# Kernel optimization log

Hardware: AMD Instinct MI355X
Metric: run time of the kernel (lower is better)

## Reference

```python
import jax, jax.numpy as jnp
import numpy as np

EPS = 1e-5

def _layernorm(h, g, b):
    mu = jnp.mean(h, axis=-1, keepdims=True)
    var = jnp.mean((h - mu) ** 2, axis=-1, keepdims=True)
    return (h - mu) / jnp.sqrt(var + EPS) * g + b

def _linoss_scan_im(A, dt, Bu):
    # A, dt: (N,) real; Bu: (B, L, N) complex64.
    # IM discretization of z' = -A x + B u, x' = z (LinOSS paper Eq. 3-4),
    # computed with a 2x2 block-diagonal associative (parallel) scan.
    S = 1.0 / (1.0 + dt * dt * A)  # Schur complement
    m11 = 1.0 - dt * dt * A * S
    m12 = -dt * A * S
    m21 = dt * S
    m22 = S
    fz = (m11 * dt) * Bu
    fx = (m21 * dt) * Bu
    Bt, L, N = Bu.shape
    br = lambda m: jnp.broadcast_to(m.astype(Bu.dtype), (Bt, L, N))
    elems = (br(m11), br(m12), br(m21), br(m22), fz, fx)

    def binop(ei, ej):
        a11i, a12i, a21i, a22i, bzi, bxi = ei
        a11j, a12j, a21j, a22j, bzj, bxj = ej
        return (a11j * a11i + a12j * a21i,
                a11j * a12i + a12j * a22i,
                a21j * a11i + a22j * a21i,
                a21j * a12i + a22j * a22i,
                a11j * bzi + a12j * bxi + bzj,
                a21j * bzi + a22j * bxi + bxj)

    res = jax.lax.associative_scan(binop, elems, axis=1)
    return res[5]  # x-component of the state, (B, L, N) complex

def setup_inputs():
    key = jax.random.key(0)
    ks = jax.random.split(key, 20)
    B, L, H_in, D_mod = 8, 2048, 128, 512
    s_in = np.float32(1.0 / np.sqrt(H_in))
    s_d = np.float32(1.0 / np.sqrt(D_mod))
    f32 = jnp.float32
    return {
        "x": jax.random.normal(ks[0], (B, L, H_in), f32),
        "W_in": jax.random.normal(ks[1], (D_mod, H_in), f32) * s_in,
        "b_in": jnp.zeros((D_mod,), f32),
        "W_enc": jax.random.normal(ks[2], (D_mod, D_mod), f32) * s_d,
        "b_enc": jnp.zeros((D_mod,), f32),
        "ln_g": jnp.ones((D_mod,), f32),
        "ln_b": jnp.zeros((D_mod,), f32),
        "A_diag": jax.random.uniform(ks[3], (D_mod,), f32),
        "log_steps": jax.random.normal(ks[4], (D_mod,), f32) * 0.5,
        "B_re": jax.random.normal(ks[5], (D_mod, D_mod), f32) * s_d,
        "B_im": jax.random.normal(ks[6], (D_mod, D_mod), f32) * s_d,
        "C_re": jax.random.normal(ks[7], (D_mod, D_mod), f32) * s_d,
        "C_im": jax.random.normal(ks[8], (D_mod, D_mod), f32) * s_d,
        "D": jax.random.normal(ks[9], (D_mod,), f32),
        "glu_w1": jax.random.normal(ks[10], (D_mod, D_mod), f32) * s_d,
        "glu_b1": jnp.zeros((D_mod,), f32),
        "glu_w2": jax.random.normal(ks[11], (D_mod, D_mod), f32) * s_d,
        "glu_b2": jnp.zeros((D_mod,), f32),
        "W_dec": jax.random.normal(ks[12], (D_mod, D_mod), f32) * s_d,
        "b_dec": jnp.zeros((D_mod,), f32),
        "W_out": jax.random.normal(ks[13], (H_in, D_mod), f32) * s_d,
        "b_out": jnp.zeros((H_in,), f32),
    }

def reference(x, W_in, b_in, W_enc, b_enc, ln_g, ln_b, A_diag, log_steps,
              B_re, B_im, C_re, C_im, D, glu_w1, glu_b1, glu_w2, glu_b2,
              W_dec, b_dec, W_out, b_out):
    h = x @ W_in.T + b_in                       # outer in_proj: (B, L, d)
    h = h @ W_enc.T + b_enc                     # LinOSS encoder
    skip = h
    hn = _layernorm(h, ln_g, ln_b)
    A = jax.nn.relu(A_diag)                     # nonnegative oscillator freqs
    dt = jax.nn.sigmoid(log_steps)              # per-state timestep in (0,1)
    Bc = (B_re + 1j * B_im).astype(jnp.complex64)
    Cc = (C_re + 1j * C_im).astype(jnp.complex64)
    Bu = jnp.einsum('blh,nh->bln', hn.astype(jnp.complex64), Bc)
    xs = _linoss_scan_im(A, dt, Bu)             # (B, L, N) complex
    y = jnp.einsum('bln,hn->blh', xs, Cc).real + D * hn
    y = jax.nn.gelu(y)
    y = (y @ glu_w1.T + glu_b1) * jax.nn.sigmoid(y @ glu_w2.T + glu_b2)  # GLU
    h = skip + y                                # residual (dropout = eval mode)
    h = h @ W_dec.T + b_dec                     # LinOSS decoder
    return h @ W_out.T + b_out                  # outer out_proj: (B, L, out)
```

## Files before the change

### kernel.cpp

```cpp
#include <hip/hip_runtime.h>
#include <cstddef>
#include <cstdint>
#include <math.h>

typedef _Float16 f16;
typedef f16 f16x8 __attribute__((ext_vector_type(8)));
typedef f16 f16x4 __attribute__((ext_vector_type(4)));
typedef float f32x4 __attribute__((ext_vector_type(4)));

constexpr int Bb   = 8;
constexpr int Ll   = 2048;
constexpr int Hin  = 128;
constexpr int Dm   = 512;
constexpr int Mrows = Bb * Ll;
constexpr int NC   = 32;
constexpr int CL   = Ll / NC;
constexpr int SZ1  = Bb * NC * Dm;
constexpr int SD   = 1024;

static __device__ __forceinline__ float sigmoid_f(float x) {
    return 1.f / (1.f + expf(-x));
}
static __device__ __forceinline__ float gelu_tanh_f(float x) {
    float x3 = x * x * x;
    float t  = tanhf(0.7978845608028654f * (x + 0.044715f * x3));
    return 0.5f * x * (1.f + t);
}

static __device__ __forceinline__ void gld16(const f16* g, f16* l) {
    __builtin_amdgcn_global_load_lds(
        (const __attribute__((address_space(1))) void*)g,
        (__attribute__((address_space(3))) void*)l, 16, 0, 0);
}

static __device__ __forceinline__ void hard_barrier() {
    __builtin_amdgcn_sched_barrier(0);
    asm volatile("s_barrier" ::: "memory");
    __builtin_amdgcn_sched_barrier(0);
}

struct CvtJob { const float* s; f16* d; int n; int lgL; int pitch; int off; int ilv; };
struct CvtJobs { CvtJob j[7]; };

__global__ __launch_bounds__(256) void prep_k(
    CvtJobs jobs,
    const float* __restrict__ Wenc, const float* __restrict__ Win,
    const float* __restrict__ b_in, const float* __restrict__ b_enc,
    const float* __restrict__ Wout, const float* __restrict__ Wdec,
    const float* __restrict__ b_dec, const float* __restrict__ b_out,
    const float* __restrict__ A_diag, const float* __restrict__ log_steps,
    const float* __restrict__ gb1, const float* __restrict__ gb2,
    f16* __restrict__ Wc1, float* __restrict__ bc1,
    f16* __restrict__ Wc2, float* __restrict__ bc2,
    float* __restrict__ cst, float* __restrict__ BG)
{
    const int y = blockIdx.y;
    if (y < 7) {
        const CvtJob jb = jobs.j[y];
        const int mask = (1 << jb.lgL) - 1;
        for (int i = (blockIdx.x * 256 + threadIdx.x) * 4; i < jb.n; i += 512 * 256 * 4) {
            const float4 v = *(const float4*)(jb.s + i);
            const int row = i >> jb.lgL;
            const int c   = i & mask;
            f16* dp = jb.ilv
                ? jb.d + (size_t)(((row >> 6) << 7) + (row & 63) + jb.off) * jb.pitch + c
                : jb.d + (size_t)row * jb.pitch + jb.off + c;
            f16x4 o;
            o.x = (f16)v.x; o.y = (f16)v.y; o.z = (f16)v.z; o.w = (f16)v.w;
            *(f16x4*)dp = o;
        }
    } else if (y == 7) {
        if (blockIdx.x >= 256) return;
        const int d2 = blockIdx.x * 2 + (threadIdx.x >> 7);
        const int t  = threadIdx.x & 127;
        float a0 = 0.f, a1 = 0.f, a2 = 0.f, a3 = 0.f;
        float a4 = 0.f, a5 = 0.f, a6 = 0.f, a7 = 0.f;
        const float* wr = Wenc + (size_t)d2 * Dm;
        for (int d = 0; d < Dm; d += 8) {
            a0 = fmaf(wr[d + 0], Win[(d + 0) * Hin + t], a0);
            a1 = fmaf(wr[d + 1], Win[(d + 1) * Hin + t], a1);
            a2 = fmaf(wr[d + 2], Win[(d + 2) * Hin + t], a2);
            a3 = fmaf(wr[d + 3], Win[(d + 3) * Hin + t], a3);
            a4 = fmaf(wr[d + 4], Win[(d + 4) * Hin + t], a4);
            a5 = fmaf(wr[d + 5], Win[(d + 5) * Hin + t], a5);
            a6 = fmaf(wr[d + 6], Win[(d + 6) * Hin + t], a6);
            a7 = fmaf(wr[d + 7], Win[(d + 7) * Hin + t], a7);
        }
        Wc1[d2 * Hin + t] = (f16)(((a0 + a1) + (a2 + a3)) + ((a4 + a5) + (a6 + a7)));
        if (t < 64) {
            float p = 0.f;
#pragma unroll
            for (int j = 0; j < 8; ++j)
                p = fmaf(wr[t + 64 * j], b_in[t + 64 * j], p);
#pragma unroll
            for (int off = 32; off > 0; off >>= 1) p += __shfl_down(p, off);
            if (t == 0) bc1[d2] = p + b_enc[d2];
        }
    } else if (y == 8) {
        if (blockIdx.x >= 128) return;
        const int o  = blockIdx.x;
        const int t0 = threadIdx.x * 2;
        const float* wo = Wout + (size_t)o * Dm;
        float x0 = 0.f, y0 = 0.f, x1 = 0.f, y1 = 0.f;
        float x2 = 0.f, y2 = 0.f, x3 = 0.f, y3 = 0.f;
        for (int d = 0; d < Dm; d += 4) {
            const float w0 = wo[d + 0], w1 = wo[d + 1], w2 = wo[d + 2], w3 = wo[d + 3];
            const float2 v0 = *(const float2*)(Wdec + (size_t)(d + 0) * Dm + t0);
            const float2 v1 = *(const float2*)(Wdec + (size_t)(d + 1) * Dm + t0);
            const float2 v2 = *(const float2*)(Wdec + (size_t)(d + 2) * Dm + t0);
            const float2 v3 = *(const float2*)(Wdec + (size_t)(d + 3) * Dm + t0);
            x0 = fmaf(w0, v0.x, x0); y0 = fmaf(w0, v0.y, y0);
            x1 = fmaf(w1, v1.x, x1); y1 = fmaf(w1, v1.y, y1);
            x2 = fmaf(w2, v2.x, x2); y2 = fmaf(w2, v2.y, y2);
            x3 = fmaf(w3, v3.x, x3); y3 = fmaf(w3, v3.y, y3);
        }
        Wc2[(size_t)o * Dm + t0]     = (f16)((x0 + x1) + (x2 + x3));
        Wc2[(size_t)o * Dm + t0 + 1] = (f16)((y0 + y1) + (y2 + y3));
        if (threadIdx.x < 64) {
            const int t = threadIdx.x;
            float p = 0.f;
#pragma unroll
            for (int j = 0; j < 8; ++j)
                p = fmaf(wo[t + 64 * j], b_dec[t + 64 * j], p);
#pragma unroll
            for (int off = 32; off > 0; off >>= 1) p += __shfl_down(p, off);
            if (t == 0) bc2[o] = p + b_out[o];
        }
    } else {
        const int n = blockIdx.x * 256 + threadIdx.x;
        if (blockIdx.x >= 2 || n >= Dm) return;
        const float a   = fmaxf(A_diag[n], 0.f);
        const float dt  = 1.f / (1.f + expf(-log_steps[n]));
        const float d2a = dt * dt * a;
        const float S   = 1.f / (1.f + d2a);
        const float m11 = 1.f - d2a * S;
        const float m12 = -dt * a * S;
        const float m21 = dt * S;
        const float m22 = S;
        cst[n]            = m11;
        cst[Dm + n]       = m12;
        cst[2 * Dm + n]   = m21;
        cst[3 * Dm + n]   = m22;
        cst[4 * Dm + n]   = m11 * dt;
        cst[5 * Dm + n]   = m21 * dt;
        const int j = n >> 6, loc = n & 63;
        BG[(j << 7) + loc]      = gb1[n];
        BG[(j << 7) + 64 + loc] = gb2[n];
    }
}

template <int KM, int OUTF16, int BM>
__global__ __launch_bounds__(256, 2) void gemm_mfma(
    const f16* __restrict__ A, const f16* __restrict__ W,
    const float* __restrict__ bias,
    const f16* __restrict__ EX, const float* __restrict__ DV,
    void* __restrict__ Cout, int M, int N, int K)
{
    constexpr int MR   = BM / 32;
    constexpr int AELE = BM * 64;
    constexpr int BELE = 128 * 64;
    __shared__ f16 smem[2 * (AELE + BELE)];

    const int tid = threadIdx.x;
    const int l   = tid & 63;
    const int wid = tid >> 6;
    const int wr  = wid >> 1;
    const int wc  = wid & 1;
    const int lc  = l & 15;
    const int lr  = l >> 4;
    const int row0 = blockIdx.x * BM;
    const int col0 = blockIdx.y * 128;

    const int NT = K >> 6;
    const int swz  = (l & 7) << 4;
    const int off0 = ((lr * 16) ^ swz) >> 1;
    const int off1 = ((64 + lr * 16) ^ swz) >> 1;

    f32x4 acc[MR][4];
#pragma unroll
    for (int i = 0; i < MR; ++i)
#pragma unroll
        for (int j = 0; j < 4; ++j) acc[i][j] = (f32x4){0.f, 0.f, 0.f, 0.f};

    auto stage_a = [&](f16* dst, const f16* src, int rs) {
#pragma unroll
        for (int c = 0; c < MR; ++c) {
            const int chunk = c * 256 + tid;
            const int row   = chunk >> 3;
            const int kb    = ((chunk & 7) << 4) ^ ((row & 7) << 4);
            gld16(src + (size_t)row * rs + (kb >> 1), dst + chunk * 8);
        }
    };
    auto stage_b = [&](f16* dst, const f16* src, int rs) {
#pragma unroll
        for (int c = 0; c < 4; ++c) {
            const int chunk = c * 256 + tid;
            const int row   = chunk >> 3;
            const int kb    = ((chunk & 7) << 4) ^ ((row & 7) << 4);
            gld16(src + (size_t)row * rs + (kb >> 1), dst + chunk * 8);
        }
    };
    auto compute = [&](const f16* As, const f16* Bs) {
#pragma unroll
        for (int ks = 0; ks < 2; ++ks) {
            const int off = ks ? off1 : off0;
            f16x8 aF[MR], bF[4];
#pragma unroll
            for (int mi = 0; mi < MR; ++mi)
                aF[mi] = *(const f16x8*)(As + (wr * (BM / 2) + mi * 16 + lc) * 64 + off);
#pragma unroll
            for (int ni = 0; ni < 4; ++ni)
                bF[ni] = *(const f16x8*)(Bs + (wc * 64 + ni * 16 + lc) * 64 + off);
#pragma unroll
            for (int mi = 0; mi < MR; ++mi)
#pragma unroll
                for (int ni = 0; ni < 4; ++ni)
                    acc[mi][ni] = __builtin_amdgcn_mfma_f32_16x16x32_f16(
                        aF[mi], bF[ni], acc[mi][ni], 0, 0, 0);
        }
    };

    stage_a(smem, A + (size_t)row0 * K, K);
    stage_b(smem + 2 * AELE, W + (size_t)col0 * K, K);
    int cur = 0;
    for (int kt = 0; kt < NT; ++kt) {
        if (kt + 1 < NT) {
            const int k1 = (kt + 1) << 6;
            stage_a(smem + (cur ^ 1) * AELE, A + (size_t)row0 * K + k1, K);
            stage_b(smem + 2 * AELE + (cur ^ 1) * BELE, W + (size_t)col0 * K + k1, K);
            if constexpr (MR == 2)      asm volatile("s_waitcnt vmcnt(6)" ::: "memory");
            else if constexpr (MR == 1) asm volatile("s_waitcnt vmcnt(5)" ::: "memory");
            else                        asm volatile("s_waitcnt vmcnt(8)" ::: "memory");
        } else {
            asm volatile("s_waitcnt vmcnt(0)" ::: "memory");
        }
        __builtin_amdgcn_sched_barrier(0);
        hard_barrier();
        compute(smem + cur * AELE, smem + 2 * AELE + cur * BELE);
        hard_barrier();
        cur ^= 1;
    }

    float* Cf32 = (float*)Cout;
    f16*   Cf16 = (f16*)Cout;
    if constexpr (KM == 5) {
        float* sig = (float*)smem;
        __syncthreads();
        if (wc == 1) {
#pragma unroll
            for (int mi = 0; mi < MR; ++mi)
#pragma unroll
                for (int ni = 0; ni < 4; ++ni) {
                    const int col = col0 + 64 + ni * 16 + lc;
                    const int rl0 = wr * (BM / 2) + mi * 16 + lr * 4;
                    const f32x4 v = acc[mi][ni];
#pragma unroll
                    for (int r = 0; r < 4; ++r)
                        sig[(rl0 + r) * 65 + ni * 16 + lc] = sigmoid_f(v[r] + bias[col]);
                }
        }
        __syncthreads();
        if (wc == 0) {
#pragma unroll
            for (int mi = 0; mi < MR; ++mi)
#pragma unroll
                for (int ni = 0; ni < 4; ++ni) {
                    const int cl   = ni * 16 + lc;
                    const int col  = col0 + cl;
                    const int hcol = blockIdx.y * 64 + cl;
                    const int rl0  = wr * (BM / 2) + mi * 16 + lr * 4;
                    const f32x4 v = acc[mi][ni];
#pragma unroll
                    for (int r = 0; r < 4; ++r) {
                        const int row = row0 + rl0 + r;
                        const float o = (float)EX[(size_t)row * Dm + hcol]
                                      + (v[r] + bias[col]) * sig[(rl0 + r) * 65 + cl];
                        Cf16[(size_t)row * Dm + hcol] = (f16)o;
                    }
                }
        }
        return;
    }
#pragma unroll
    for (int mi = 0; mi < MR; ++mi) {
#pragma unroll
        for (int ni = 0; ni < 4; ++ni) {
            const int col   = col0 + wc * 64 + ni * 16 + lc;
            const int rbase = row0 + wr * (BM / 2) + mi * 16 + lr * 4;
            const f32x4 v = acc[mi][ni];
            if (KM == 1) {
                const float dv = DV[col];
#pragma unroll
                for (int r = 0; r < 4; ++r) {
                    const size_t idx = (size_t)(rbase + r) * N + col;
                    const float o = gelu_tanh_f(v[r] + dv * (float)EX[idx]);
                    if (OUTF16) Cf16[idx] = (f16)o; else Cf32[idx] = o;
                }
            } else {
                const float bv = bias ? bias[col] : 0.f;
#pragma unroll
                for (int r = 0; r < 4; ++r) {
                    const float o = v[r] + bv;
                    const size_t idx = (size_t)(rbase + r) * N + col;
                    if (OUTF16) Cf16[idx] = (f16)o; else Cf32[idx] = o;
                }
            }
        }
    }
}

__global__ __launch_bounds__(256) void layernorm_f16(
    const f16* __restrict__ X, const float* __restrict__ g,
    const float* __restrict__ b, f16* __restrict__ Y)
{
    const int lane = threadIdx.x & 63;
    const int w    = threadIdx.x >> 6;
    const int row  = blockIdx.x * 4 + w;
    const size_t base = (size_t)row * Dm + lane * 8;

    const f16x8 v = *(const f16x8*)(X + base);
    float x[8];
    float s = 0.f, q = 0.f;
#pragma unroll
    for (int i = 0; i < 8; ++i) {
        x[i] = (float)v[i];
        s += x[i]; q += x[i] * x[i];
    }
#pragma unroll
    for (int off = 32; off > 0; off >>= 1) {
        s += __shfl_xor(s, off);
        q += __shfl_xor(q, off);
    }
    const float mu  = s * (1.f / 512.f);
    const float var = q * (1.f / 512.f) - mu * mu;
    const float rs  = rsqrtf(var + 1e-5f);

    const float4 g0 = *(const float4*)(g + lane * 8);
    const float4 g1 = *(const float4*)(g + lane * 8 + 4);
    const float4 b0 = *(const float4*)(b + lane * 8);
    const float4 b1 = *(const float4*)(b + lane * 8 + 4);
    const float gg[8] = {g0.x, g0.y, g0.z, g0.w, g1.x, g1.y, g1.z, g1.w};
    const float bb[8] = {b0.x, b0.y, b0.z, b0.w, b1.x, b1.y, b1.z, b1.w};
    f16x8 o;
#pragma unroll
    for (int i = 0; i < 8; ++i)
        o[i] = (f16)((x[i] - mu) * rs * gg[i] + bb[i]);
    *(f16x8*)(Y + base) = o;
}

__global__ __launch_bounds__(512) void scan_phase1(
    const f16* __restrict__ BU, const float* __restrict__ cst,
    float* __restrict__ S1)
{
    const int n = threadIdx.x;
    const int c = blockIdx.x & (NC - 1);
    const int b = blockIdx.x >> 5;
    const float m11 = cst[n],          m12 = cst[Dm + n];
    const float m21 = cst[2 * Dm + n], m22 = cst[3 * Dm + n];
    const float c1  = cst[4 * Dm + n], c2  = cst[5 * Dm + n];

    float zr = 0.f, xr = 0.f, zi = 0.f, xi = 0.f;
    const size_t base = ((size_t)b * Ll + (size_t)c * CL) * SD + n;
#pragma unroll 4
    for (int t = 0; t < CL; ++t) {
        const float br = (float)BU[base + (size_t)t * SD];
        const float bi = (float)BU[base + (size_t)t * SD + 512];
        const float zrn = fmaf(m11, zr, fmaf(m12, xr, c1 * br));
        const float xrn = fmaf(m21, zr, fmaf(m22, xr, c2 * br));
        const float zin = fmaf(m11, zi, fmaf(m12, xi, c1 * bi));
        const float xin = fmaf(m21, zi, fmaf(m22, xi, c2 * bi));
        zr = zrn; xr = xrn; zi = zin; xi = xin;
    }
    const int idx = blockIdx.x * Dm + n;
    S1[idx]            = zr;
    S1[SZ1 + idx]      = xr;
    S1[2 * SZ1 + idx]  = zi;
    S1[3 * SZ1 + idx]  = xi;
}

__global__ __launch_bounds__(256) void scan_phase2(
    const float* __restrict__ S1, const float* __restrict__ cst,
    float* __restrict__ G)
{
    const int gidx = blockIdx.x * 256 + threadIdx.x;
    const int n = gidx & (Dm - 1);
    const int b = gidx >> 9;
    const float m11 = cst[n],          m12 = cst[Dm + n];
    const float m21 = cst[2 * Dm + n], m22 = cst[3 * Dm + n];

    float p11 = 1.f, p12 = 0.f, p21 = 0.f, p22 = 1.f;
    for (int i = 0; i < CL; ++i) {
        const float q11 = m11 * p11 + m12 * p21;
        const float q12 = m11 * p12 + m12 * p22;
        const float q21 = m21 * p11 + m22 * p21;
        const float q22 = m21 * p12 + m22 * p22;
        p11 = q11; p12 = q12; p21 = q21; p22 = q22;
    }

    float gzr = 0.f, gxr = 0.f, gzi = 0.f, gxi = 0.f;
    for (int c = 0; c < NC; ++c) {
        const int idx = (b * NC + c) * Dm + n;
        G[idx]           = gzr;
        G[SZ1 + idx]     = gxr;
        G[2 * SZ1 + idx] = gzi;
        G[3 * SZ1 + idx] = gxi;
        const float szr = S1[idx],           sxr = S1[SZ1 + idx];
        const float szi = S1[2 * SZ1 + idx], sxi = S1[3 * SZ1 + idx];
        const float t1 = p11 * gzr + p12 * gxr + szr;
        const float t2 = p21 * gzr + p22 * gxr + sxr;
        const float t3 = p11 * gzi + p12 * gxi + szi;
        const float t4 = p21 * gzi + p22 * gxi + sxi;
        gzr = t1; gxr = t2; gzi = t3; gxi = t4;
    }
}

__global__ __launch_bounds__(512) void scan_phase3(
    const f16* __restrict__ BU, const float* __restrict__ cst,
    const float* __restrict__ G, f16* __restrict__ XS)
{
    const int n = threadIdx.x;
    const int c = blockIdx.x & (NC - 1);
    const int b = blockIdx.x >> 5;
    const float m11 = cst[n],          m12 = cst[Dm + n];
    const float m21 = cst[2 * Dm + n], m22 = cst[3 * Dm + n];
    const float c1  = cst[4 * Dm + n], c2  = cst[5 * Dm + n];

    const int sidx = blockIdx.x * Dm + n;
    float zr = G[sidx];
    float xr = G[SZ1 + sidx];
    float zi = G[2 * SZ1 + sidx];
    float xi = G[3 * SZ1 + sidx];

    const size_t base = ((size_t)b * Ll + (size_t)c * CL) * SD + n;
#pragma unroll 4
    for (int t = 0; t < CL; ++t) {
        const float br = (float)BU[base + (size_t)t * SD];
        const float bi = (float)BU[base + (size_t)t * SD + 512];
        const float zrn = fmaf(m11, zr, fmaf(m12, xr, c1 * br));
        const float xrn = fmaf(m21, zr, fmaf(m22, xr, c2 * br));
        const float zin = fmaf(m11, zi, fmaf(m12, xi, c1 * bi));
        const float xin = fmaf(m21, zi, fmaf(m22, xi, c2 * bi));
        zr = zrn; xr = xrn; zi = zin; xi = xin;
        XS[base + (size_t)t * SD]       = (f16)xr;
        XS[base + (size_t)t * SD + 512] = (f16)(-xi);
    }
}

extern "C" void kernel_launch(void* const* d_in, const int* in_sizes, int n_in,
                              void* d_out, int out_size, void* d_ws, size_t ws_size,
                              hipStream_t stream)
{
    const float* x         = (const float*)d_in[0];
    const float* W_in      = (const float*)d_in[1];
    const float* b_in      = (const float*)d_in[2];
    const float* W_enc     = (const float*)d_in[3];
    const float* b_enc     = (const float*)d_in[4];
    const float* ln_g      = (const float*)d_in[5];
    const float* ln_b      = (const float*)d_in[6];
    const float* A_diag    = (const float*)d_in[7];
    const float* log_steps = (const float*)d_in[8];
    const float* B_re      = (const float*)d_in[9];
    const float* B_im      = (const float*)d_in[10];
    const float* C_re      = (const float*)d_in[11];
    const float* C_im      = (const float*)d_in[12];
    const float* Dv        = (const float*)d_in[13];
    const float* glu_w1    = (const float*)d_in[14];
    const float* glu_b1    = (const float*)d_in[15];
    const float* glu_w2    = (const float*)d_in[16];
    const float* glu_b2    = (const float*)d_in[17];
    const float* W_dec     = (const float*)d_in[18];
    const float* b_dec     = (const float*)d_in[19];
    const float* W_out     = (const float*)d_in[20];
    const float* b_out     = (const float*)d_in[21];

    char* ws = (char*)d_ws;
    const size_t MB = 1 << 20;
    f16*   F2  = (f16*)(ws);
    f16*   F3  = (f16*)(ws + 16 * MB);
    f16*   XS  = (f16*)(ws + 32 * MB);
    f16*   BU  = (f16*)(ws + 64 * MB);
    f16*   GF  = (f16*)(ws + 96 * MB);
    f16*   XF  = (f16*)(ws + 112 * MB);
    float* S1  = (float*)(ws + 116 * MB);
    float* G   = (float*)(ws + 118 * MB);
    float* cst = (float*)(ws + 120 * MB);
    float* BG  = (float*)(ws + 120 * MB + 64 * 1024);
    float* bc1 = (float*)(ws + 120 * MB + 128 * 1024);
    float* bc2 = (float*)(ws + 120 * MB + 192 * 1024);
    f16*   WB  = (f16*)(ws + 121 * MB);
    f16*   WC  = (f16*)(ws + 122 * MB);
    f16*   WG  = (f16*)(ws + 123 * MB);
    f16*   Wc1 = (f16*)(ws + 124 * MB);
    f16*   Wc2 = (f16*)(ws + 124 * MB + 256 * 1024);

    CvtJobs jobs;
    jobs.j[0] = {x,      XF,            Mrows * Hin, 7, Hin,  0,   0};
    jobs.j[1] = {B_re,   WB,            Dm * Dm,     9, Dm,   0,   0};
    jobs.j[2] = {B_im,   WB + 512 * Dm, Dm * Dm,     9, Dm,   0,   0};
    jobs.j[3] = {C_re,   WC,            Dm * Dm,     9, 1024, 0,   0};
    jobs.j[4] = {C_im,   WC,            Dm * Dm,     9, 1024, 512, 0};
    jobs.j[5] = {glu_w1, WG,            Dm * Dm,     9, Dm,   0,   1};
    jobs.j[6] = {glu_w2, WG,            Dm * Dm,     9, Dm,   64,  1};

    prep_k<<<dim3(512, 10), 256, 0, stream>>>(
        jobs, W_enc, W_in, b_in, b_enc, W_out, W_dec, b_dec, b_out,
        A_diag, log_steps, glu_b1, glu_b2, Wc1, bc1, Wc2, bc2, cst, BG);

    dim3 blk(256);

    gemm_mfma<0, 1, 64><<<dim3(Mrows / 64, 4), blk, 0, stream>>>(
        XF, Wc1, bc1, nullptr, nullptr, F2, Mrows, Dm, Hin);
    layernorm_f16<<<Mrows / 4, 256, 0, stream>>>(F2, ln_g, ln_b, F3);
    gemm_mfma<0, 1, 64><<<dim3(Mrows / 64, 8), blk, 0, stream>>>(
        F3, WB, nullptr, nullptr, nullptr, BU, Mrows, 1024, Dm);
    scan_phase1<<<Bb * NC, 512, 0, stream>>>(BU, cst, S1);
    scan_phase2<<<(Bb * Dm) / 256, 256, 0, stream>>>(S1, cst, G);
    scan_phase3<<<Bb * NC, 512, 0, stream>>>(BU, cst, G, XS);
    gemm_mfma<1, 1, 64><<<dim3(Mrows / 64, 4), blk, 0, stream>>>(
        XS, WC, nullptr, F3, Dv, GF, Mrows, Dm, 1024);
    gemm_mfma<5, 1, 64><<<dim3(Mrows / 64, 8), blk, 0, stream>>>(
        GF, WG, BG, F2, nullptr, F3, Mrows, 1024, Dm);
    gemm_mfma<0, 0, 32><<<dim3(Mrows / 32, 1), blk, 0, stream>>>(
        F3, Wc2, bc2, nullptr, nullptr, (float*)d_out, Mrows, Hin, Dm);
}
```

Measured before the change: 297.0 us.

## Compute fused weight products with MFMA GEMMs and double scan chunk count

The W_enc·W_in and W_out·W_dec weight pre-products were computed with scalar FMA loops inside the prep kernel. They are now done by converting the weights to f16 (transposing W_in and W_dec through LDS tiles) and running two small MFMA GEMM launches. Separately, the scan chunk count doubles from 32 to 64, which gives the scan phases twice as many blocks with shorter serial chunks. The cost is two extra kernel launches, f16 rounding of the intermediate weight products, and a larger chunk-carry workspace for phase 2.

```diff
diff --git a/kernel.cpp b/kernel.cpp
--- a/kernel.cpp
+++ b/kernel.cpp
@@ -13,7 +13,7 @@
 constexpr int Hin  = 128;
 constexpr int Dm   = 512;
 constexpr int Mrows = Bb * Ll;
-constexpr int NC   = 32;
+constexpr int NC   = 64;
 constexpr int CL   = Ll / NC;
 constexpr int SZ1  = Bb * NC * Dm;
 constexpr int SD   = 1024;
@@ -40,7 +40,7 @@
 }
 
 struct CvtJob { const float* s; f16* d; int n; int lgL; int pitch; int off; int ilv; };
-struct CvtJobs { CvtJob j[7]; };
+struct CvtJobs { CvtJob j[9]; };
 
 __global__ __launch_bounds__(256) void prep_k(
     CvtJobs jobs,
@@ -50,12 +50,13 @@
     const float* __restrict__ b_dec, const float* __restrict__ b_out,
     const float* __restrict__ A_diag, const float* __restrict__ log_steps,
     const float* __restrict__ gb1, const float* __restrict__ gb2,
-    f16* __restrict__ Wc1, float* __restrict__ bc1,
-    f16* __restrict__ Wc2, float* __restrict__ bc2,
+    f16* __restrict__ WinT, f16* __restrict__ WdecT,
+    float* __restrict__ bc1, float* __restrict__ bc2,
     float* __restrict__ cst, float* __restrict__ BG)
 {
+    __shared__ float tile[64][65];
     const int y = blockIdx.y;
-    if (y < 7) {
+    if (y < 9) {
         const CvtJob jb = jobs.j[y];
         const int mask = (1 << jb.lgL) - 1;
         for (int i = (blockIdx.x * 256 + threadIdx.x) * 4; i < jb.n; i += 512 * 256 * 4) {
@@ -69,64 +70,59 @@
             o.x = (f16)v.x; o.y = (f16)v.y; o.z = (f16)v.z; o.w = (f16)v.w;
             *(f16x4*)dp = o;
         }
-    } else if (y == 7) {
-        if (blockIdx.x >= 256) return;
-        const int d2 = blockIdx.x * 2 + (threadIdx.x >> 7);
-        const int t  = threadIdx.x & 127;
-        float a0 = 0.f, a1 = 0.f, a2 = 0.f, a3 = 0.f;
-        float a4 = 0.f, a5 = 0.f, a6 = 0.f, a7 = 0.f;
-        const float* wr = Wenc + (size_t)d2 * Dm;
-        for (int d = 0; d < Dm; d += 8) {
-            a0 = fmaf(wr[d + 0], Win[(d + 0) * Hin + t], a0);
-            a1 = fmaf(wr[d + 1], Win[(d + 1) * Hin + t], a1);
-            a2 = fmaf(wr[d + 2], Win[(d + 2) * Hin + t], a2);
-            a3 = fmaf(wr[d + 3], Win[(d + 3) * Hin + t], a3);
-            a4 = fmaf(wr[d + 4], Win[(d + 4) * Hin + t], a4);
-            a5 = fmaf(wr[d + 5], Win[(d + 5) * Hin + t], a5);
-            a6 = fmaf(wr[d + 6], Win[(d + 6) * Hin + t], a6);
-            a7 = fmaf(wr[d + 7], Win[(d + 7) * Hin + t], a7);
-        }
-        Wc1[d2 * Hin + t] = (f16)(((a0 + a1) + (a2 + a3)) + ((a4 + a5) + (a6 + a7)));
-        if (t < 64) {
+    } else if (y == 9 || y == 10) {
+        const int LW   = (y == 9) ? Hin : Dm;
+        const float* S = (y == 9) ? Win : Wdec;
+        f16* D         = (y == 9) ? WinT : WdecT;
+        const int NTIL = (y == 9) ? 16 : 64;
+        const int CT   = LW >> 6;
+        if (blockIdx.x >= NTIL) return;
+        const int tr = blockIdx.x / CT, tc = blockIdx.x % CT;
+        const int r0 = tr * 64, c0 = tc * 64;
+        const int tid = threadIdx.x;
+#pragma unroll
+        for (int i = 0; i < 4; ++i) {
+            const int r  = (tid >> 4) + i * 16;
+            const int c4 = (tid & 15) * 4;
+            const float4 v = *(const float4*)(S + (size_t)(r0 + r) * LW + c0 + c4);
+            tile[r][c4 + 0] = v.x; tile[r][c4 + 1] = v.y;
+            tile[r][c4 + 2] = v.z; tile[r][c4 + 3] = v.w;
+        }
+        __syncthreads();
+#pragma unroll
+        for (int i = 0; i < 4; ++i) {
+            const int c  = (tid >> 4) + i * 16;
+            const int r4 = (tid & 15) * 4;
+            f16x4 o;
+            o.x = (f16)tile[r4 + 0][c]; o.y = (f16)tile[r4 + 1][c];
+            o.z = (f16)tile[r4 + 2][c]; o.w = (f16)tile[r4 + 3][c];
+            *(f16x4*)(D + (size_t)(c0 + c) * 512 + r0 + r4) = o;
+        }
+    } else if (y == 11) {
+        const int w    = threadIdx.x >> 6;
+        const int lane = threadIdx.x & 63;
+        if (blockIdx.x < 128) {
+            const int d2 = blockIdx.x * 4 + w;
+            const float* wr = Wenc + (size_t)d2 * Dm;
             float p = 0.f;
 #pragma unroll
             for (int j = 0; j < 8; ++j)
-                p = fmaf(wr[t + 64 * j], b_in[t + 64 * j], p);
+                p = fmaf(wr[lane + 64 * j], b_in[lane + 64 * j], p);
 #pragma unroll
             for (int off = 32; off > 0; off >>= 1) p += __shfl_down(p, off);
-            if (t == 0) bc1[d2] = p + b_enc[d2];
-        }
-    } else if (y == 8) {
-        if (blockIdx.x >= 128) return;
-        const int o  = blockIdx.x;
-        const int t0 = threadIdx.x * 2;
-        const float* wo = Wout + (size_t)o * Dm;
-        float x0 = 0.f, y0 = 0.f, x1 = 0.f, y1 = 0.f;
-        float x2 = 0.f, y2 = 0.f, x3 = 0.f, y3 = 0.f;
-        for (int d = 0; d < Dm; d += 4) {
-            const float w0 = wo[d + 0], w1 = wo[d + 1], w2 = wo[d + 2], w3 = wo[d + 3];
-            const float2 v0 = *(const float2*)(Wdec + (size_t)(d + 0) * Dm + t0);
-            const float2 v1 = *(const float2*)(Wdec + (size_t)(d + 1) * Dm + t0);
-            const float2 v2 = *(const float2*)(Wdec + (size_t)(d + 2) * Dm + t0);
-            const float2 v3 = *(const float2*)(Wdec + (size_t)(d + 3) * Dm + t0);
-            x0 = fmaf(w0, v0.x, x0); y0 = fmaf(w0, v0.y, y0);
-            x1 = fmaf(w1, v1.x, x1); y1 = fmaf(w1, v1.y, y1);
-            x2 = fmaf(w2, v2.x, x2); y2 = fmaf(w2, v2.y, y2);
-            x3 = fmaf(w3, v3.x, x3); y3 = fmaf(w3, v3.y, y3);
-        }
-        Wc2[(size_t)o * Dm + t0]     = (f16)((x0 + x1) + (x2 + x3));
-        Wc2[(size_t)o * Dm + t0 + 1] = (f16)((y0 + y1) + (y2 + y3));
-        if (threadIdx.x < 64) {
-            const int t = threadIdx.x;
+            if (lane == 0) bc1[d2] = p + b_enc[d2];
+        } else if (blockIdx.x < 160) {
+            const int o = (blockIdx.x - 128) * 4 + w;
+            const float* wo = Wout + (size_t)o * Dm;
             float p = 0.f;
 #pragma unroll
             for (int j = 0; j < 8; ++j)
-                p = fmaf(wo[t + 64 * j], b_dec[t + 64 * j], p);
+                p = fmaf(wo[lane + 64 * j], b_dec[lane + 64 * j], p);
 #pragma unroll
             for (int off = 32; off > 0; off >>= 1) p += __shfl_down(p, off);
-            if (t == 0) bc2[o] = p + b_out[o];
-        }
-    } else {
+            if (lane == 0) bc2[o] = p + b_out[o];
+        }
+    } else if (y == 12) {
         const int n = blockIdx.x * 256 + threadIdx.x;
         if (blockIdx.x >= 2 || n >= Dm) return;
         const float a   = fmaxf(A_diag[n], 0.f);
@@ -354,7 +350,7 @@
 {
     const int n = threadIdx.x;
     const int c = blockIdx.x & (NC - 1);
-    const int b = blockIdx.x >> 5;
+    const int b = blockIdx.x >> 6;
     const float m11 = cst[n],          m12 = cst[Dm + n];
     const float m21 = cst[2 * Dm + n], m22 = cst[3 * Dm + n];
     const float c1  = cst[4 * Dm + n], c2  = cst[5 * Dm + n];
@@ -420,7 +416,7 @@
 {
     const int n = threadIdx.x;
     const int c = blockIdx.x & (NC - 1);
-    const int b = blockIdx.x >> 5;
+    const int b = blockIdx.x >> 6;
     const float m11 = cst[n],          m12 = cst[Dm + n];
     const float m21 = cst[2 * Dm + n], m22 = cst[3 * Dm + n];
     const float c1  = cst[4 * Dm + n], c2  = cst[5 * Dm + n];
@@ -475,6 +471,7 @@
 
     char* ws = (char*)d_ws;
     const size_t MB = 1 << 20;
+    const size_t KB = 1 << 10;
     f16*   F2  = (f16*)(ws);
     f16*   F3  = (f16*)(ws + 16 * MB);
     f16*   XS  = (f16*)(ws + 32 * MB);
@@ -482,16 +479,20 @@
     f16*   GF  = (f16*)(ws + 96 * MB);
     f16*   XF  = (f16*)(ws + 112 * MB);
     float* S1  = (float*)(ws + 116 * MB);
-    float* G   = (float*)(ws + 118 * MB);
-    float* cst = (float*)(ws + 120 * MB);
-    float* BG  = (float*)(ws + 120 * MB + 64 * 1024);
-    float* bc1 = (float*)(ws + 120 * MB + 128 * 1024);
-    float* bc2 = (float*)(ws + 120 * MB + 192 * 1024);
-    f16*   WB  = (f16*)(ws + 121 * MB);
-    f16*   WC  = (f16*)(ws + 122 * MB);
-    f16*   WG  = (f16*)(ws + 123 * MB);
-    f16*   Wc1 = (f16*)(ws + 124 * MB);
-    f16*   Wc2 = (f16*)(ws + 124 * MB + 256 * 1024);
+    float* G   = (float*)(ws + 120 * MB);
+    float* cst = (float*)(ws + 124 * MB);
+    float* BG  = (float*)(ws + 124 * MB + 64 * KB);
+    float* bc1 = (float*)(ws + 124 * MB + 128 * KB);
+    float* bc2 = (float*)(ws + 124 * MB + 192 * KB);
+    f16*   WB  = (f16*)(ws + 125 * MB);
+    f16*   WC  = (f16*)(ws + 126 * MB);
+    f16*   WG  = (f16*)(ws + 127 * MB);
+    f16*   Wc1   = (f16*)(ws + 128 * MB);
+    f16*   Wc2   = (f16*)(ws + 128 * MB + 128 * KB);
+    f16*   WinT  = (f16*)(ws + 128 * MB + 256 * KB);
+    f16*   WoutF = (f16*)(ws + 128 * MB + 384 * KB);
+    f16*   WencF = (f16*)(ws + 128 * MB + 512 * KB);
+    f16*   WdecT = (f16*)(ws + 129 * MB);
 
     CvtJobs jobs;
     jobs.j[0] = {x,      XF,            Mrows * Hin, 7, Hin,  0,   0};
@@ -501,12 +502,19 @@
     jobs.j[4] = {C_im,   WC,            Dm * Dm,     9, 1024, 512, 0};
     jobs.j[5] = {glu_w1, WG,            Dm * Dm,     9, Dm,   0,   1};
     jobs.j[6] = {glu_w2, WG,            Dm * Dm,     9, Dm,   64,  1};
-
-    prep_k<<<dim3(512, 10), 256, 0, stream>>>(
+    jobs.j[7] = {W_enc,  WencF,         Dm * Dm,     9, Dm,   0,   0};
+    jobs.j[8] = {W_out,  WoutF,         Hin * Dm,    9, Dm,   0,   0};
+
+    prep_k<<<dim3(512, 13), 256, 0, stream>>>(
         jobs, W_enc, W_in, b_in, b_enc, W_out, W_dec, b_dec, b_out,
-        A_diag, log_steps, glu_b1, glu_b2, Wc1, bc1, Wc2, bc2, cst, BG);
+        A_diag, log_steps, glu_b1, glu_b2, WinT, WdecT, bc1, bc2, cst, BG);
 
     dim3 blk(256);
+
+    gemm_mfma<0, 1, 64><<<dim3(8, 1), blk, 0, stream>>>(
+        WencF, WinT, nullptr, nullptr, nullptr, Wc1, 512, 128, 512);
+    gemm_mfma<0, 1, 64><<<dim3(2, 4), blk, 0, stream>>>(
+        WoutF, WdecT, nullptr, nullptr, nullptr, Wc2, 128, 512, 512);
 
     gemm_mfma<0, 1, 64><<<dim3(Mrows / 64, 4), blk, 0, stream>>>(
         XF, Wc1, bc1, nullptr, nullptr, F2, Mrows, Dm, Hin);
```

Result: faster. 277.3 us (-6.6%).
